# Kernel tuning notes

Hardware: AMD Instinct MI355X
Metric: run time of the kernel (lower is better)

Reference implementation:

```python
import jax, jax.numpy as jnp
import numpy as np

EPS = 1e-5
N_HEADS = 16
TOP_K = 2


def _ln(x, g, b):
    m = x.mean(-1, keepdims=True)
    v = ((x - m) ** 2).mean(-1, keepdims=True)
    return (x - m) / jnp.sqrt(v + EPS) * g + b


def _block_fwd(x, ln1_g, ln1_b, ln2_g, ln2_b, Wq, bq, Wk, bk, Wv, bv, Wo, bo,
               Wr, br, e_w1, e_b1, e_w2, e_b2):
    B, S, D = x.shape
    H = N_HEADS
    hd = D // H
    # --- LN + causal MHA + residual (dropout is identity at eval) ---
    h = _ln(x, ln1_g, ln1_b)
    q = (h @ Wq + bq).reshape(B, S, H, hd).transpose(0, 2, 1, 3)  # [B,H,S,hd]
    k = (h @ Wk + bk).reshape(B, S, H, hd).transpose(0, 2, 1, 3)
    v = (h @ Wv + bv).reshape(B, S, H, hd).transpose(0, 2, 1, 3)
    scores = jnp.einsum('bhqd,bhkd->bhqk', q, k) / (hd ** 0.5)
    causal = jnp.tril(jnp.ones((S, S), dtype=bool))
    scores = jnp.where(causal, scores, -jnp.inf)
    attn = jax.nn.softmax(scores, axis=-1)
    o = jnp.einsum('bhqk,bhkd->bhqd', attn, v).transpose(0, 2, 1, 3).reshape(B, S, D)
    a = (o @ Wo + bo) + x
    # --- LN + dense-computed SparseMoE + residual ---
    h2 = _ln(a, ln2_g, ln2_b)
    logits = h2 @ Wr + br                         # [B,S,E]
    topv = jax.lax.top_k(logits, TOP_K)[0]        # [B,S,K]
    kmask = logits >= topv[..., -1:]
    w = jax.nn.softmax(jnp.where(kmask, logits, -jnp.inf), axis=-1)  # [B,S,E]
    # dense per-expert FFN, exactly as the torch module computes it
    mid = jax.nn.gelu(jnp.einsum('bsd,edf->bsef', h2, e_w1) + e_b1,
                      approximate=False)          # [B,S,E,4D]
    eo = jnp.einsum('bsef,efd->bsed', mid, e_w2) + e_b2  # [B,S,E,D]
    moe = jnp.einsum('bse,bsed->bsd', w, eo)
    return moe + a


def setup_inputs() -> dict:
    key = jax.random.key(0)
    B, S, D, E = 1, 2048, 1024, 8
    F = 4 * D
    ks = jax.random.split(key, 8)

    def n(k, shape):
        return jax.random.normal(k, shape, jnp.float32) * 0.02

    return dict(
        x=jax.random.normal(ks[0], (B, S, D), jnp.float32),
        ln1_g=jnp.ones((D,), jnp.float32), ln1_b=jnp.zeros((D,), jnp.float32),
        ln2_g=jnp.ones((D,), jnp.float32), ln2_b=jnp.zeros((D,), jnp.float32),
        Wq=n(ks[1], (D, D)), bq=jnp.zeros((D,), jnp.float32),
        Wk=n(ks[2], (D, D)), bk=jnp.zeros((D,), jnp.float32),
        Wv=n(ks[3], (D, D)), bv=jnp.zeros((D,), jnp.float32),
        Wo=n(ks[4], (D, D)), bo=jnp.zeros((D,), jnp.float32),
        Wr=n(ks[5], (D, E)), br=jnp.zeros((E,), jnp.float32),
        e_w1=n(ks[6], (E, D, F)), e_b1=jnp.zeros((E, F), jnp.float32),
        e_w2=n(ks[7], (E, F, D)), e_b2=jnp.zeros((E, D), jnp.float32),
    )


def reference(x, ln1_g, ln1_b, ln2_g, ln2_b, Wq, bq, Wk, bk, Wv, bv, Wo, bo,
              Wr, br, e_w1, e_b1, e_w2, e_b2):
    return _block_fwd(x, ln1_g, ln1_b, ln2_g, ln2_b, Wq, bq, Wk, bk, Wv, bv,
                      Wo, bo, Wr, br, e_w1, e_b1, e_w2, e_b2)
```

## Files before the change

### kernel.cpp

```cpp
#include <hip/hip_runtime.h>
#include <hip/hip_bf16.h>
#include <math.h>

#define S 2048
#define Dm 1024
#define Ee 8
#define Ff 4096

typedef __attribute__((ext_vector_type(8))) short bf16x8;
typedef __attribute__((ext_vector_type(4))) float f32x4;

__device__ __forceinline__ unsigned short f2bf(float f) {
    union { float f; unsigned int u; } c; c.f = f;
    unsigned int r = (c.u + 0x7fffu + ((c.u >> 16) & 1u)) >> 16;
    return (unsigned short)r;
}

__device__ __forceinline__ float bf2f(unsigned short u) {
    union { float f; unsigned int i; } c; c.i = ((unsigned int)u) << 16; return c.f;
}

__device__ __forceinline__ void gload16(const void* g, void* l) {
    __builtin_amdgcn_global_load_lds(
        (const __attribute__((address_space(1))) void*)g,
        (__attribute__((address_space(3))) void*)l, 16, 0, 0);
}

__device__ __forceinline__ float gelu_f(float x) {
    float ax = fabsf(x) * 0.70710678118654752f;
    float t = 1.0f / (1.0f + 0.3275911f * ax);
    float p = t * (0.254829592f + t * (-0.284496736f + t * (1.421413741f +
              t * (-1.453152027f + t * 1.061405429f))));
    float er = 1.0f - p * __expf(-ax * ax);
    er = (x < 0.0f) ? -er : er;
    return 0.5f * x * (1.0f + er);
}

__global__ __launch_bounds__(256) void ln_kernel(const float* __restrict__ x,
                                                 const float* __restrict__ g,
                                                 const float* __restrict__ b,
                                                 unsigned short* __restrict__ obf) {
    int row = blockIdx.x;
    int tid = threadIdx.x;
    float4 v = ((const float4*)(x + (size_t)row * Dm))[tid];
    float s  = v.x + v.y + v.z + v.w;
    float sq = v.x*v.x + v.y*v.y + v.z*v.z + v.w*v.w;
    #pragma unroll
    for (int off = 1; off < 64; off <<= 1) {
        s  += __shfl_xor(s, off);
        sq += __shfl_xor(sq, off);
    }
    __shared__ float ps[4], pq[4];
    int wave = tid >> 6;
    if ((tid & 63) == 0) { ps[wave] = s; pq[wave] = sq; }
    __syncthreads();
    s  = ps[0] + ps[1] + ps[2] + ps[3];
    sq = pq[0] + pq[1] + pq[2] + pq[3];
    float mean = s * (1.0f / Dm);
    float var  = sq * (1.0f / Dm) - mean * mean;
    float rstd = rsqrtf(var + 1e-5f);
    float4 gv = ((const float4*)g)[tid];
    float4 bv = ((const float4*)b)[tid];
    float4 o;
    o.x = (v.x - mean) * rstd * gv.x + bv.x;
    o.y = (v.y - mean) * rstd * gv.y + bv.y;
    o.z = (v.z - mean) * rstd * gv.z + bv.z;
    o.w = (v.w - mean) * rstd * gv.w + bv.w;
    unsigned short t4[4] = { f2bf(o.x), f2bf(o.y), f2bf(o.z), f2bf(o.w) };
    *(uint2*)(obf + (size_t)row * Dm + tid * 4) = *(uint2*)t4;
}

__global__ __launch_bounds__(256) void ln2_fused(const float* __restrict__ x,
                                                 const float* __restrict__ p0,
                                                 const float* __restrict__ p1,
                                                 const float* __restrict__ bo,
                                                 const float* __restrict__ g,
                                                 const float* __restrict__ b,
                                                 const float* __restrict__ Wr,
                                                 const float* __restrict__ br,
                                                 float* __restrict__ aout,
                                                 unsigned short* __restrict__ h2b,
                                                 float* __restrict__ w_rt) {
    int row = blockIdx.x;
    int tid = threadIdx.x;
    size_t base = (size_t)row * Dm;
    float4 xv = ((const float4*)(x + base))[tid];
    float4 a0 = ((const float4*)(p0 + base))[tid];
    float4 a1 = ((const float4*)(p1 + base))[tid];
    float4 bv0 = ((const float4*)bo)[tid];
    float4 a;
    a.x = xv.x + a0.x + a1.x + bv0.x;
    a.y = xv.y + a0.y + a1.y + bv0.y;
    a.z = xv.z + a0.z + a1.z + bv0.z;
    a.w = xv.w + a0.w + a1.w + bv0.w;
    ((float4*)(aout + base))[tid] = a;
    float s  = a.x + a.y + a.z + a.w;
    float sq = a.x*a.x + a.y*a.y + a.z*a.z + a.w*a.w;
    #pragma unroll
    for (int off = 1; off < 64; off <<= 1) {
        s  += __shfl_xor(s, off);
        sq += __shfl_xor(sq, off);
    }
    __shared__ float ps[4], pq[4];
    int wave = tid >> 6;
    if ((tid & 63) == 0) { ps[wave] = s; pq[wave] = sq; }
    __syncthreads();
    s  = ps[0] + ps[1] + ps[2] + ps[3];
    sq = pq[0] + pq[1] + pq[2] + pq[3];
    float mean = s * (1.0f / Dm);
    float var  = sq * (1.0f / Dm) - mean * mean;
    float rstd = rsqrtf(var + 1e-5f);
    float4 gv = ((const float4*)g)[tid];
    float4 bbv = ((const float4*)b)[tid];
    float4 o;
    o.x = (a.x - mean) * rstd * gv.x + bbv.x;
    o.y = (a.y - mean) * rstd * gv.y + bbv.y;
    o.z = (a.z - mean) * rstd * gv.z + bbv.z;
    o.w = (a.w - mean) * rstd * gv.w + bbv.w;
    unsigned short t4[4] = { f2bf(o.x), f2bf(o.y), f2bf(o.z), f2bf(o.w) };
    *(uint2*)(h2b + base + tid * 4) = *(uint2*)t4;

    float lg[8];
    #pragma unroll
    for (int e = 0; e < 8; e++) lg[e] = 0.0f;
    float oc[4] = { o.x, o.y, o.z, o.w };
    #pragma unroll
    for (int c = 0; c < 4; c++) {
        const float4* wr4 = (const float4*)(Wr + (size_t)(tid * 4 + c) * Ee);
        float4 wa = wr4[0], wb = wr4[1];
        lg[0] += oc[c]*wa.x; lg[1] += oc[c]*wa.y; lg[2] += oc[c]*wa.z; lg[3] += oc[c]*wa.w;
        lg[4] += oc[c]*wb.x; lg[5] += oc[c]*wb.y; lg[6] += oc[c]*wb.z; lg[7] += oc[c]*wb.w;
    }
    #pragma unroll
    for (int e = 0; e < 8; e++)
        #pragma unroll
        for (int off = 1; off < 64; off <<= 1) lg[e] += __shfl_xor(lg[e], off);
    __shared__ float wlg[4][8];
    if ((tid & 63) == 0) {
        #pragma unroll
        for (int e = 0; e < 8; e++) wlg[wave][e] = lg[e];
    }
    __syncthreads();
    if (tid == 0) {
        float l8[8];
        #pragma unroll
        for (int e = 0; e < 8; e++) l8[e] = wlg[0][e] + wlg[1][e] + wlg[2][e] + wlg[3][e] + br[e];
        float v1 = -INFINITY, v2 = -INFINITY;
        for (int e = 0; e < 8; e++) {
            float xv2 = l8[e];
            if (xv2 > v1) { v2 = v1; v1 = xv2; }
            else if (xv2 > v2) v2 = xv2;
        }
        float wv[8]; float denom = 0.0f;
        for (int e = 0; e < 8; e++) {
            if (l8[e] >= v2) { wv[e] = __expf(l8[e] - v1); denom += wv[e]; }
            else wv[e] = 0.0f;
        }
        float inv = 1.0f / denom;
        for (int e = 0; e < 8; e++) w_rt[row * Ee + e] = wv[e] * inv;
    }
}

__global__ __launch_bounds__(256) void tconv(const float* __restrict__ src,
                                             unsigned short* __restrict__ dst,
                                             int Kk, int Nn) {
    src += (size_t)blockIdx.z * Kk * Nn;
    dst += (size_t)blockIdx.z * Kk * Nn;
    int n0 = blockIdx.x * 64, k0 = blockIdx.y * 64;
    int tid = threadIdx.x;
    __shared__ float t[64][65];
    #pragma unroll
    for (int p = 0; p < 4; p++) {
        int kr = p * 16 + (tid >> 4);
        int nc = (tid & 15) * 4;
        float4 v = *(const float4*)(src + (size_t)(k0 + kr) * Nn + n0 + nc);
        t[kr][nc] = v.x; t[kr][nc+1] = v.y; t[kr][nc+2] = v.z; t[kr][nc+3] = v.w;
    }
    __syncthreads();
    int nr = tid >> 2;
    int kc = (tid & 3) * 16;
    unsigned short o[16];
    #pragma unroll
    for (int j = 0; j < 16; j++) o[j] = f2bf(t[kc + j][nr]);
    *(bf16x8*)(dst + (size_t)(n0 + nr) * Kk + k0 + kc)     = *(bf16x8*)&o[0];
    *(bf16x8*)(dst + (size_t)(n0 + nr) * Kk + k0 + kc + 8) = *(bf16x8*)&o[8];
}

template<int MODE>
__global__ __launch_bounds__(256, 2) void gemm_db(const unsigned short* __restrict__ A,
                                                  const unsigned short* __restrict__ Wt,
                                                  const float* __restrict__ bias0,
                                                  const float* __restrict__ bias1,
                                                  const float* __restrict__ bias2,
                                                  void* __restrict__ Cout,
                                                  int M, int N, int K) {
    const int tid = threadIdx.x;
    const int lane = tid & 63;
    const int w = tid >> 6;
    const int lr = lane >> 4, lc = lane & 15;
    const int wr = w >> 1, wc = w & 1;

    int kc = (MODE == 1) ? blockIdx.z : 0;
    const int m0 = blockIdx.y * 128;
    const int n0 = blockIdx.x * 128;
    const int KL   = (MODE == 1) ? 512 : K;
    const int Koff = kc * KL;

    __shared__ __align__(16) unsigned short As[2][128 * 64];
    __shared__ __align__(16) unsigned short Bs[2][128 * 64];

    const int srow = lane >> 3;
    const int csw  = ((lane & 7) ^ srow) * 8;
    const unsigned short* asrc[4];
    const unsigned short* bsrc[4];
    #pragma unroll
    for (int i = 0; i < 4; i++) {
        int rl = w * 32 + i * 8 + srow;
        asrc[i] = A  + (size_t)(m0 + rl) * K + Koff + csw;
        bsrc[i] = Wt + (size_t)(n0 + rl) * K + Koff + csw;
    }

    f32x4 acc[4][4];
    #pragma unroll
    for (int a = 0; a < 4; a++)
        #pragma unroll
        for (int bb = 0; bb < 4; bb++) acc[a][bb] = (f32x4)0.0f;

    auto STAGE = [&](int buf, int kblk) {
        const size_t koff = (size_t)kblk * 64;
        #pragma unroll
        for (int i = 0; i < 4; i++) {
            gload16(asrc[i] + koff, &As[buf][(w * 32 + i * 8) * 64]);
            gload16(bsrc[i] + koff, &Bs[buf][(w * 32 + i * 8) * 64]);
        }
    };

    const int nt = KL / 64;
    STAGE(0, 0);
    for (int t = 0; t < nt; ++t) {
        const int cur = t & 1;
        if (t + 1 < nt) {
            STAGE(cur ^ 1, t + 1);
            asm volatile("s_waitcnt vmcnt(8)" ::: "memory");
        } else {
            asm volatile("s_waitcnt vmcnt(0)" ::: "memory");
        }
        __builtin_amdgcn_s_barrier();
        #pragma unroll
        for (int ks = 0; ks < 2; ks++) {
            const int ck = ((ks * 4 + lr) ^ (lc & 7)) * 8;
            bf16x8 af[4], bfv[4];
            #pragma unroll
            for (int fm = 0; fm < 4; fm++)
                af[fm] = *(const bf16x8*)&As[cur][(wr * 64 + fm * 16 + lc) * 64 + ck];
            #pragma unroll
            for (int fn = 0; fn < 4; fn++)
                bfv[fn] = *(const bf16x8*)&Bs[cur][(wc * 64 + fn * 16 + lc) * 64 + ck];
            #pragma unroll
            for (int fm = 0; fm < 4; fm++)
                #pragma unroll
                for (int fn = 0; fn < 4; fn++)
                    acc[fm][fn] = __builtin_amdgcn_mfma_f32_16x16x32_bf16(af[fm], bfv[fn], acc[fm][fn], 0, 0, 0);
        }
        asm volatile("" ::: "memory");
        __builtin_amdgcn_s_barrier();
    }

    #pragma unroll
    for (int fm = 0; fm < 4; fm++) {
        #pragma unroll
        for (int r = 0; r < 4; r++) {
            int m = m0 + wr * 64 + fm * 16 + lr * 4 + r;
            #pragma unroll
            for (int fn = 0; fn < 4; fn++) {
                int ncol = n0 + wc * 64 + fn * 16 + lc;
                float val = acc[fm][fn][r];
                if constexpr (MODE == 0) {
                    const float* bb = (ncol < 1024) ? bias0 : (ncol < 2048 ? bias1 : bias2);
                    val += bb[ncol & 1023];
                    ((unsigned short*)Cout)[(size_t)m * N + ncol] = f2bf(val);
                } else {
                    ((float*)Cout)[(size_t)kc * M * N + (size_t)m * N + ncol] = val;
                }
            }
        }
    }
}

template<int MODE>
__global__ __launch_bounds__(256, 4) void gemm_moe(const unsigned short* __restrict__ A,
                                                   const unsigned short* __restrict__ Wt,
                                                   const float* __restrict__ bias,
                                                   void* __restrict__ Cout,
                                                   const int* __restrict__ rows,
                                                   const int* __restrict__ counts,
                                                   const int* __restrict__ offs,
                                                   const int* __restrict__ tilemap,
                                                   const int* __restrict__ ntiles,
                                                   int N, int K) {
    const int by = blockIdx.y;
    if (by >= *ntiles) return;
    const int tm = tilemap[by];
    const int e  = tm >> 8;
    const int m0 = (tm & 255) * 128;
    const int kc = (MODE == 3) ? blockIdx.z : 0;

    const int tid = threadIdx.x;
    const int lane = tid & 63;
    const int w = tid >> 6;
    const int lr = lane >> 4, lc = lane & 15;
    const int wr = w >> 1, wc = w & 1;

    const int Mcnt = counts[e];
    const int n0 = blockIdx.x * 128;
    const int KL = (MODE == 3) ? (K >> 2) : K;
    const int Koff = kc * KL;
    const unsigned short* Wz = Wt + (size_t)e * N * K;
    const float* biasz = bias + (size_t)e * N;
    const int zoff = offs[e];

    __shared__ __align__(16) unsigned short As[128 * 64];
    __shared__ __align__(16) unsigned short Bs[128 * 64];

    const int srow = lane >> 3;
    const int csw  = ((lane & 7) ^ srow) * 8;
    const unsigned short* asrc[4];
    const unsigned short* bsrc[4];
    #pragma unroll
    for (int i = 0; i < 4; i++) {
        int rl = w * 32 + i * 8 + srow;
        int ma = m0 + rl;
        int srcRow;
        if constexpr (MODE == 2) srcRow = rows[e * S + (ma < Mcnt ? ma : Mcnt - 1)];
        else                     srcRow = zoff + (ma < Mcnt ? ma : Mcnt - 1);
        asrc[i] = A  + (size_t)srcRow * K + Koff + csw;
        bsrc[i] = Wz + (size_t)(n0 + rl) * K + Koff + csw;
    }

    f32x4 acc[4][4];
    #pragma unroll
    for (int a = 0; a < 4; a++)
        #pragma unroll
        for (int bb = 0; bb < 4; bb++) acc[a][bb] = (f32x4)0.0f;

    for (int k0 = 0; k0 < KL; k0 += 64) {
        #pragma unroll
        for (int i = 0; i < 4; i++) {
            gload16(asrc[i] + k0, &As[(w * 32 + i * 8) * 64]);
            gload16(bsrc[i] + k0, &Bs[(w * 32 + i * 8) * 64]);
        }
        __syncthreads();
        #pragma unroll
        for (int ks = 0; ks < 2; ks++) {
            const int ck = ((ks * 4 + lr) ^ (lc & 7)) * 8;
            bf16x8 af[4], bfv[4];
            #pragma unroll
            for (int fm = 0; fm < 4; fm++)
                af[fm] = *(const bf16x8*)&As[(wr * 64 + fm * 16 + lc) * 64 + ck];
            #pragma unroll
            for (int fn = 0; fn < 4; fn++)
                bfv[fn] = *(const bf16x8*)&Bs[(wc * 64 + fn * 16 + lc) * 64 + ck];
            #pragma unroll
            for (int fm = 0; fm < 4; fm++)
                #pragma unroll
                for (int fn = 0; fn < 4; fn++)
                    acc[fm][fn] = __builtin_amdgcn_mfma_f32_16x16x32_bf16(af[fm], bfv[fn], acc[fm][fn], 0, 0, 0);
        }
        __syncthreads();
    }

    #pragma unroll
    for (int fm = 0; fm < 4; fm++) {
        #pragma unroll
        for (int r = 0; r < 4; r++) {
            int m = m0 + wr * 64 + fm * 16 + lr * 4 + r;
            if (m >= Mcnt) continue;
            #pragma unroll
            for (int fn = 0; fn < 4; fn++) {
                int ncol = n0 + wc * 64 + fn * 16 + lc;
                float val = acc[fm][fn][r];
                if constexpr (MODE == 2) {
                    val += biasz[ncol];
                    ((unsigned short*)Cout)[(size_t)(zoff + m) * N + ncol] = f2bf(gelu_f(val));
                } else {
                    if (kc == 0) val += biasz[ncol];
                    ((unsigned short*)Cout)[(size_t)kc * 4096 * N + (size_t)(zoff + m) * N + ncol] = f2bf(val);
                }
            }
        }
    }
}

__global__ __launch_bounds__(256) void attn_mfma(const unsigned short* __restrict__ qkv,
                                                 unsigned short* __restrict__ ob) {
    int bid = blockIdx.x;
    int qt, h;
    if (bid < 256) { qt = 31 - (bid & 31); h = bid >> 5; }
    else           { qt = bid & 31;        h = 8 + ((bid - 256) >> 5); }
    int tid = threadIdx.x;
    int lane = tid & 63, w = tid >> 6;
    int lr = lane >> 4, lc = lane & 15;

    __shared__ __align__(16) unsigned short Kl[2][64 * 64];
    __shared__ __align__(16) unsigned short Vt[2][64 * 64];
    __shared__ __align__(16) unsigned short Pl[4][16 * 64];

    bf16x8 qf[2];
    int qg_base = qt * 64 + w * 16;
    {
        int qrow = qg_base + lc;
        #pragma unroll
        for (int ks = 0; ks < 2; ks++)
            qf[ks] = *(const bf16x8*)(qkv + (size_t)qrow * 3072 + h * 64 + ks * 32 + lr * 8);
    }

    const int srow = lane >> 3;
    const int scw  = ((lane & 7) ^ srow) * 8;
    const unsigned short* ksrc[2];
    #pragma unroll
    for (int i = 0; i < 2; i++)
        ksrc[i] = qkv + (size_t)(w * 16 + i * 8 + srow) * 3072 + h * 64 + 1024 + scw;
    int vrow[2], vcg[2];
    const unsigned short* vsrc[2];
    #pragma unroll
    for (int i = 0; i < 2; i++) {
        int u = tid + i * 256;
        vrow[i] = u >> 3; vcg[i] = (u & 7) * 8;
        vsrc[i] = qkv + (size_t)vrow[i] * 3072 + h * 64 + 2048 + vcg[i];
    }

    f32x4 oacc[4];
    #pragma unroll
    for (int fd = 0; fd < 4; fd++) oacc[fd] = (f32x4)0.0f;
    float mrun[4], lrun[4];
    #pragma unroll
    for (int r = 0; r < 4; r++) { mrun[r] = -INFINITY; lrun[r] = 0.0f; }

    bf16x8 vreg[2];
    vreg[0] = *(const bf16x8*)(vsrc[0]);
    vreg[1] = *(const bf16x8*)(vsrc[1]);
    gload16(ksrc[0], &Kl[0][(w * 16 + 0) * 64]);
    gload16(ksrc[1], &Kl[0][(w * 16 + 8) * 64]);
    #pragma unroll
    for (int i = 0; i < 2; i++)
        #pragma unroll
        for (int j = 0; j < 8; j++) {
            int d = vcg[i] + j;
            int ch = ((vrow[i] >> 3) ^ (d & 7) ^ (d >> 3)) & 7;
            Vt[0][d * 64 + ch * 8 + (vrow[i] & 7)] = (unsigned short)vreg[i][j];
        }
    __syncthreads();

    for (int kt = 0; kt <= qt; kt++) {
        const int cur = kt & 1;
        if (kt < qt) {
            size_t off = (size_t)(kt + 1) * 64 * 3072;
            vreg[0] = *(const bf16x8*)(vsrc[0] + off);
            vreg[1] = *(const bf16x8*)(vsrc[1] + off);
            gload16(ksrc[0] + off, &Kl[cur ^ 1][(w * 16 + 0) * 64]);
            gload16(ksrc[1] + off, &Kl[cur ^ 1][(w * 16 + 8) * 64]);
        }

        f32x4 sc[4];
        #pragma unroll
        for (int fn = 0; fn < 4; fn++) sc[fn] = (f32x4)0.0f;
        __builtin_amdgcn_s_setprio(1);
        #pragma unroll
        for (int fn = 0; fn < 4; fn++)
            #pragma unroll
            for (int ks = 0; ks < 2; ks++) {
                bf16x8 kf = *(const bf16x8*)&Kl[cur][(fn * 16 + lc) * 64 + ((ks * 4 + lr) ^ (lc & 7)) * 8];
                sc[fn] = __builtin_amdgcn_mfma_f32_16x16x32_bf16(qf[ks], kf, sc[fn], 0, 0, 0);
            }
        __builtin_amdgcn_s_setprio(0);

        float st[4][4];
        float mloc[4];
        #pragma unroll
        for (int r = 0; r < 4; r++) mloc[r] = -INFINITY;
        #pragma unroll
        for (int fn = 0; fn < 4; fn++)
            #pragma unroll
            for (int r = 0; r < 4; r++) {
                float sv = sc[fn][r] * 0.125f;
                if (kt == qt) {
                    int kvg = kt * 64 + fn * 16 + lc;
                    int qg  = qg_base + lr * 4 + r;
                    if (kvg > qg) sv = -INFINITY;
                }
                st[fn][r] = sv;
                mloc[r] = fmaxf(mloc[r], sv);
            }
        #pragma unroll
        for (int r = 0; r < 4; r++) {
            mloc[r] = fmaxf(mloc[r], __shfl_xor(mloc[r], 1));
            mloc[r] = fmaxf(mloc[r], __shfl_xor(mloc[r], 2));
            mloc[r] = fmaxf(mloc[r], __shfl_xor(mloc[r], 4));
            mloc[r] = fmaxf(mloc[r], __shfl_xor(mloc[r], 8));
        }
        float fsc[4], lpart[4];
        #pragma unroll
        for (int r = 0; r < 4; r++) {
            float mnew = fmaxf(mrun[r], mloc[r]);
            fsc[r] = __expf(mrun[r] - mnew);
            mrun[r] = mnew;
            lpart[r] = 0.0f;
        }
        float pv[4][4];
        #pragma unroll
        for (int fn = 0; fn < 4; fn++)
            #pragma unroll
            for (int r = 0; r < 4; r++) {
                pv[fn][r] = __expf(st[fn][r] - mrun[r]);
                lpart[r] += pv[fn][r];
            }
        #pragma unroll
        for (int r = 0; r < 4; r++) {
            lpart[r] += __shfl_xor(lpart[r], 1);
            lpart[r] += __shfl_xor(lpart[r], 2);
            lpart[r] += __shfl_xor(lpart[r], 4);
            lpart[r] += __shfl_xor(lpart[r], 8);
            lrun[r] = lrun[r] * fsc[r] + lpart[r];
        }
        #pragma unroll
        for (int fn = 0; fn < 4; fn++)
            #pragma unroll
            for (int r = 0; r < 4; r++) {
                int q = lr * 4 + r;
                int kvc = fn * 16 + lc;
                int ch = ((kvc >> 3) ^ (q & 7) ^ (q >> 3)) & 7;
                Pl[w][q * 64 + ch * 8 + (kvc & 7)] = f2bf(pv[fn][r]);
            }
        #pragma unroll
        for (int fd = 0; fd < 4; fd++)
            #pragma unroll
            for (int r = 0; r < 4; r++) oacc[fd][r] *= fsc[r];

        if (kt < qt) {
            #pragma unroll
            for (int i = 0; i < 2; i++)
                #pragma unroll
                for (int j = 0; j < 8; j++) {
                    int d = vcg[i] + j;
                    int ch = ((vrow[i] >> 3) ^ (d & 7) ^ (d >> 3)) & 7;
                    Vt[cur ^ 1][d * 64 + ch * 8 + (vrow[i] & 7)] = (unsigned short)vreg[i][j];
                }
        }

        __builtin_amdgcn_s_setprio(1);
        #pragma unroll
        for (int ks = 0; ks < 2; ks++) {
            int chp = ((ks * 4 + lr) ^ (lc & 7) ^ (lc >> 3)) & 7;
            bf16x8 pa = *(const bf16x8*)&Pl[w][lc * 64 + chp * 8];
            #pragma unroll
            for (int fd = 0; fd < 4; fd++) {
                int d = fd * 16 + lc;
                int chv = ((ks * 4 + lr) ^ (d & 7) ^ (d >> 3)) & 7;
                bf16x8 vb = *(const bf16x8*)&Vt[cur][d * 64 + chv * 8];
                oacc[fd] = __builtin_amdgcn_mfma_f32_16x16x32_bf16(pa, vb, oacc[fd], 0, 0, 0);
            }
        }
        __builtin_amdgcn_s_setprio(0);
        __syncthreads();
    }
    #pragma unroll
    for (int fd = 0; fd < 4; fd++)
        #pragma unroll
        for (int r = 0; r < 4; r++) {
            float val = oacc[fd][r] / lrun[r];
            ob[(size_t)(qg_base + lr * 4 + r) * 1024 + h * 64 + fd * 16 + lc] = f2bf(val);
        }
}

__global__ __launch_bounds__(256) void listbuild_kernel(const float* __restrict__ w_rt,
                                                        int* __restrict__ rows,
                                                        int* __restrict__ counts,
                                                        int* __restrict__ offs,
                                                        int* __restrict__ tok2slot,
                                                        float* __restrict__ tokw,
                                                        int* __restrict__ tilemap,
                                                        int* __restrict__ ntiles) {
    int tid = threadIdx.x;
    __shared__ int sc[256];
    __shared__ int runoff_s;
    __shared__ int scounts[8];
    int ncnt[8];
    #pragma unroll
    for (int j = 0; j < 8; j++) ncnt[j] = 0;
    if (tid == 0) runoff_s = 0;
    __syncthreads();
    for (int e = 0; e < Ee; e++) {
        int t0 = tid * 8;
        int sel = 0, flags = 0;
        #pragma unroll
        for (int j = 0; j < 8; j++)
            if (w_rt[(size_t)(t0 + j) * Ee + e] > 0.0f) { flags |= 1 << j; sel++; }
        sc[tid] = sel;
        __syncthreads();
        for (int off = 1; off < 256; off <<= 1) {
            int add = (tid >= off) ? sc[tid - off] : 0;
            __syncthreads();
            sc[tid] += add;
            __syncthreads();
        }
        int base = runoff_s;
        int pos = sc[tid] - sel;
        #pragma unroll
        for (int j = 0; j < 8; j++) {
            if (flags & (1 << j)) {
                rows[e * S + pos] = t0 + j;
                int c = ncnt[j];
                if (c < 2) {
                    tok2slot[(t0 + j) * 2 + c] = base + pos;
                    tokw[(t0 + j) * 2 + c] = w_rt[(size_t)(t0 + j) * Ee + e];
                    ncnt[j] = c + 1;
                }
                pos++;
            }
        }
        __syncthreads();
        if (tid == 0) {
            offs[e] = base;
            counts[e] = sc[255];
            scounts[e] = sc[255];
            runoff_s = base + sc[255];
        }
        __syncthreads();
    }
    if (tid == 0) {
        int t = 0;
        for (int e = 0; e < Ee; e++) {
            int nmt = (scounts[e] + 127) >> 7;
            for (int mt = 0; mt < nmt; mt++) tilemap[t++] = (e << 8) | mt;
        }
        *ntiles = t;
        for (int j = t; j < 40; j++) tilemap[j] = 0;
    }
}

__global__ __launch_bounds__(256) void combine_kernel(float* __restrict__ out,
                                                      const unsigned short* __restrict__ eo,
                                                      const int* __restrict__ tok2slot,
                                                      const float* __restrict__ tokw) {
    int t = blockIdx.x, d = threadIdx.x;
    int s0 = tok2slot[t * 2], s1 = tok2slot[t * 2 + 1];
    float w0 = tokw[t * 2], w1 = tokw[t * 2 + 1];
    float4 o = ((const float4*)(out + (size_t)t * Dm))[d];
    float a[4] = {0,0,0,0}, b[4] = {0,0,0,0};
    #pragma unroll
    for (int p = 0; p < 4; p++) {
        const unsigned short* ep = eo + (size_t)p * 4096 * Dm;
        uint2 ra = *(const uint2*)(ep + (size_t)s0 * Dm + d * 4);
        uint2 rb = *(const uint2*)(ep + (size_t)s1 * Dm + d * 4);
        const unsigned short* pa16 = (const unsigned short*)&ra;
        const unsigned short* pb16 = (const unsigned short*)&rb;
        #pragma unroll
        for (int j = 0; j < 4; j++) { a[j] += bf2f(pa16[j]); b[j] += bf2f(pb16[j]); }
    }
    o.x += w0 * a[0] + w1 * b[0];
    o.y += w0 * a[1] + w1 * b[1];
    o.z += w0 * a[2] + w1 * b[2];
    o.w += w0 * a[3] + w1 * b[3];
    ((float4*)(out + (size_t)t * Dm))[d] = o;
}

extern "C" void kernel_launch(void* const* d_in, const int* in_sizes, int n_in,
                              void* d_out, int out_size, void* d_ws, size_t ws_size,
                              hipStream_t stream) {
    const float* x    = (const float*)d_in[0];
    const float* ln1g = (const float*)d_in[1];
    const float* ln1b = (const float*)d_in[2];
    const float* ln2g = (const float*)d_in[3];
    const float* ln2b = (const float*)d_in[4];
    const float* Wq   = (const float*)d_in[5];
    const float* bq   = (const float*)d_in[6];
    const float* Wk   = (const float*)d_in[7];
    const float* bk   = (const float*)d_in[8];
    const float* Wv   = (const float*)d_in[9];
    const float* bv   = (const float*)d_in[10];
    const float* Wo   = (const float*)d_in[11];
    const float* bo   = (const float*)d_in[12];
    const float* Wr   = (const float*)d_in[13];
    const float* br   = (const float*)d_in[14];
    const float* ew1  = (const float*)d_in[15];
    const float* eb1  = (const float*)d_in[16];
    const float* ew2  = (const float*)d_in[17];
    const float* eb2  = (const float*)d_in[18];
    float* out = (float*)d_out;

    char* wsb = (char*)d_ws;
    const size_t MB = 1 << 20;
    unsigned short* ew1T = (unsigned short*)(wsb);
    unsigned short* eo   = (unsigned short*)(wsb);
    unsigned short* ew2T = (unsigned short*)(wsb + 64*MB);
    unsigned short* mid  = (unsigned short*)(wsb + 128*MB);
    unsigned short* qkvT = (unsigned short*)(wsb + 160*MB);
    unsigned short* WoT  = (unsigned short*)(wsb + 166*MB);
    unsigned short* h_bf = (unsigned short*)(wsb + 168*MB);
    unsigned short* qkv  = (unsigned short*)(wsb + 172*MB);
    float*          p01  = (float*)         (wsb + 168*MB);
    unsigned short* ob   = (unsigned short*)(wsb + 184*MB);
    unsigned short* h2b  = (unsigned short*)(wsb + 196*MB);
    float*          w_rt = (float*)         (wsb + 200*MB);
    int*            rows = (int*)           (wsb + 200*MB + 65536);
    int*            counts   = rows + Ee * S;
    int*            offs     = counts + Ee;
    int*            tok2slot = offs + Ee;
    float*          tokw     = (float*)(tok2slot + 2 * S);
    int*            tilemap  = (int*)(tokw + 2 * S);
    int*            ntiles   = tilemap + 40;

    tconv<<<dim3(16, 16, 1), 256, 0, stream>>>(Wq, qkvT,               Dm, Dm);
    tconv<<<dim3(16, 16, 1), 256, 0, stream>>>(Wk, qkvT + 1024*1024,   Dm, Dm);
    tconv<<<dim3(16, 16, 1), 256, 0, stream>>>(Wv, qkvT + 2*1024*1024, Dm, Dm);
    tconv<<<dim3(16, 16, 1), 256, 0, stream>>>(Wo, WoT,                Dm, Dm);
    tconv<<<dim3(64, 16, 8), 256, 0, stream>>>(ew1, ew1T, Dm, Ff);
    tconv<<<dim3(16, 64, 8), 256, 0, stream>>>(ew2, ew2T, Ff, Dm);

    ln_kernel<<<S, 256, 0, stream>>>(x, ln1g, ln1b, h_bf);

    gemm_db<0><<<dim3(24, 16), 256, 0, stream>>>(h_bf, qkvT, bq, bk, bv,
        qkv, S, 3072, Dm);

    attn_mfma<<<dim3(512, 1), 256, 0, stream>>>(qkv, ob);

    gemm_db<1><<<dim3(8, 16, 2), 256, 0, stream>>>(ob, WoT, nullptr, nullptr, nullptr,
        p01, S, Dm, Dm);

    ln2_fused<<<S, 256, 0, stream>>>(x, p01, p01 + (size_t)S * Dm, bo, ln2g, ln2b,
                                     Wr, br, out, h2b, w_rt);
    listbuild_kernel<<<1, 256, 0, stream>>>(w_rt, rows, counts, offs, tok2slot, tokw,
                                            tilemap, ntiles);

    gemm_moe<2><<<dim3(32, 40, 1), 256, 0, stream>>>(h2b, ew1T, eb1,
        mid, rows, counts, offs, tilemap, ntiles, Ff, Dm);

    gemm_moe<3><<<dim3(8, 40, 4), 256, 0, stream>>>(mid, ew2T, eb2,
        eo, rows, counts, offs, tilemap, ntiles, Dm, Ff);

    combine_kernel<<<S, 256, 0, stream>>>(out, eo, tok2slot, tokw);
}
```

Baseline: 377.0 us.

## Halve MoE GEMM K-tile to raise occupancy and batch weight transposes

The MoE GEMM kernel now stages 32-wide K tiles instead of 64-wide. This halves its LDS footprint, and the launch bound is raised to 6 blocks per CU so more blocks can be resident and hide latency. The cost is twice as many K-loop iterations and barriers per tile. The four attention weight transpose/convert launches are also merged into one kernel launch with a z-dimension of 4, which cuts launch overhead.

```diff
diff --git a/kernel.cpp b/kernel.cpp
--- a/kernel.cpp
+++ b/kernel.cpp
@@ -186,6 +186,35 @@
     *(bf16x8*)(dst + (size_t)(n0 + nr) * Kk + k0 + kc + 8) = *(bf16x8*)&o[8];
 }
 
+__global__ __launch_bounds__(256) void tconv4(const float* __restrict__ s0,
+                                              const float* __restrict__ s1,
+                                              const float* __restrict__ s2,
+                                              const float* __restrict__ s3,
+                                              unsigned short* __restrict__ d0,
+                                              unsigned short* __restrict__ d3) {
+    int z = blockIdx.z;
+    const float* src = (z == 0) ? s0 : (z == 1 ? s1 : (z == 2 ? s2 : s3));
+    unsigned short* dst = (z < 3) ? d0 + (size_t)z * 1024 * 1024 : d3;
+    int n0 = blockIdx.x * 64, k0 = blockIdx.y * 64;
+    int tid = threadIdx.x;
+    __shared__ float t[64][65];
+    #pragma unroll
+    for (int p = 0; p < 4; p++) {
+        int kr = p * 16 + (tid >> 4);
+        int nc = (tid & 15) * 4;
+        float4 v = *(const float4*)(src + (size_t)(k0 + kr) * 1024 + n0 + nc);
+        t[kr][nc] = v.x; t[kr][nc+1] = v.y; t[kr][nc+2] = v.z; t[kr][nc+3] = v.w;
+    }
+    __syncthreads();
+    int nr = tid >> 2;
+    int kc = (tid & 3) * 16;
+    unsigned short o[16];
+    #pragma unroll
+    for (int j = 0; j < 16; j++) o[j] = f2bf(t[kc + j][nr]);
+    *(bf16x8*)(dst + (size_t)(n0 + nr) * 1024 + k0 + kc)     = *(bf16x8*)&o[0];
+    *(bf16x8*)(dst + (size_t)(n0 + nr) * 1024 + k0 + kc + 8) = *(bf16x8*)&o[8];
+}
+
 template<int MODE>
 __global__ __launch_bounds__(256, 2) void gemm_db(const unsigned short* __restrict__ A,
                                                   const unsigned short* __restrict__ Wt,
@@ -288,7 +317,7 @@
 }
 
 template<int MODE>
-__global__ __launch_bounds__(256, 4) void gemm_moe(const unsigned short* __restrict__ A,
+__global__ __launch_bounds__(256, 6) void gemm_moe(const unsigned short* __restrict__ A,
                                                    const unsigned short* __restrict__ Wt,
                                                    const float* __restrict__ bias,
                                                    void* __restrict__ Cout,
@@ -319,16 +348,16 @@
     const float* biasz = bias + (size_t)e * N;
     const int zoff = offs[e];
 
-    __shared__ __align__(16) unsigned short As[128 * 64];
-    __shared__ __align__(16) unsigned short Bs[128 * 64];
-
-    const int srow = lane >> 3;
-    const int csw  = ((lane & 7) ^ srow) * 8;
-    const unsigned short* asrc[4];
-    const unsigned short* bsrc[4];
-    #pragma unroll
-    for (int i = 0; i < 4; i++) {
-        int rl = w * 32 + i * 8 + srow;
+    __shared__ __align__(16) unsigned short As[128 * 32];
+    __shared__ __align__(16) unsigned short Bs[128 * 32];
+
+    const int srow = lane >> 2;
+    const int csw  = ((lane & 3) ^ (srow & 3)) * 8;
+    const unsigned short* asrc[2];
+    const unsigned short* bsrc[2];
+    #pragma unroll
+    for (int i = 0; i < 2; i++) {
+        int rl = (w * 2 + i) * 16 + srow;
         int ma = m0 + rl;
         int srcRow;
         if constexpr (MODE == 2) srcRow = rows[e * S + (ma < Mcnt ? ma : Mcnt - 1)];
@@ -343,29 +372,27 @@
         #pragma unroll
         for (int bb = 0; bb < 4; bb++) acc[a][bb] = (f32x4)0.0f;
 
-    for (int k0 = 0; k0 < KL; k0 += 64) {
-        #pragma unroll
-        for (int i = 0; i < 4; i++) {
-            gload16(asrc[i] + k0, &As[(w * 32 + i * 8) * 64]);
-            gload16(bsrc[i] + k0, &Bs[(w * 32 + i * 8) * 64]);
+    const int ckr = (lr ^ (lc & 3)) * 8;
+
+    for (int k0 = 0; k0 < KL; k0 += 32) {
+        #pragma unroll
+        for (int i = 0; i < 2; i++) {
+            gload16(asrc[i] + k0, &As[((w * 2 + i) * 16) * 32]);
+            gload16(bsrc[i] + k0, &Bs[((w * 2 + i) * 16) * 32]);
         }
         __syncthreads();
-        #pragma unroll
-        for (int ks = 0; ks < 2; ks++) {
-            const int ck = ((ks * 4 + lr) ^ (lc & 7)) * 8;
-            bf16x8 af[4], bfv[4];
-            #pragma unroll
-            for (int fm = 0; fm < 4; fm++)
-                af[fm] = *(const bf16x8*)&As[(wr * 64 + fm * 16 + lc) * 64 + ck];
+        bf16x8 af[4], bfv[4];
+        #pragma unroll
+        for (int fm = 0; fm < 4; fm++)
+            af[fm] = *(const bf16x8*)&As[(wr * 64 + fm * 16 + lc) * 32 + ckr];
+        #pragma unroll
+        for (int fn = 0; fn < 4; fn++)
+            bfv[fn] = *(const bf16x8*)&Bs[(wc * 64 + fn * 16 + lc) * 32 + ckr];
+        #pragma unroll
+        for (int fm = 0; fm < 4; fm++)
             #pragma unroll
             for (int fn = 0; fn < 4; fn++)
-                bfv[fn] = *(const bf16x8*)&Bs[(wc * 64 + fn * 16 + lc) * 64 + ck];
-            #pragma unroll
-            for (int fm = 0; fm < 4; fm++)
-                #pragma unroll
-                for (int fn = 0; fn < 4; fn++)
-                    acc[fm][fn] = __builtin_amdgcn_mfma_f32_16x16x32_bf16(af[fm], bfv[fn], acc[fm][fn], 0, 0, 0);
-        }
+                acc[fm][fn] = __builtin_amdgcn_mfma_f32_16x16x32_bf16(af[fm], bfv[fn], acc[fm][fn], 0, 0, 0);
         __syncthreads();
     }
 
@@ -710,10 +737,7 @@
     int*            tilemap  = (int*)(tokw + 2 * S);
     int*            ntiles   = tilemap + 40;
 
-    tconv<<<dim3(16, 16, 1), 256, 0, stream>>>(Wq, qkvT,               Dm, Dm);
-    tconv<<<dim3(16, 16, 1), 256, 0, stream>>>(Wk, qkvT + 1024*1024,   Dm, Dm);
-    tconv<<<dim3(16, 16, 1), 256, 0, stream>>>(Wv, qkvT + 2*1024*1024, Dm, Dm);
-    tconv<<<dim3(16, 16, 1), 256, 0, stream>>>(Wo, WoT,                Dm, Dm);
+    tconv4<<<dim3(16, 16, 4), 256, 0, stream>>>(Wq, Wk, Wv, Wo, qkvT, WoT);
     tconv<<<dim3(64, 16, 8), 256, 0, stream>>>(ew1, ew1T, Dm, Ff);
     tconv<<<dim3(16, 64, 8), 256, 0, stream>>>(ew2, ew2T, Ff, Dm);
 
```

New measurement: 815.2 us. 116% more time.
